# Performance work log

Measured on AMD Instinct MI355X. Metric: run time of the kernel, lower is better.

## Reference

```python
import jax, jax.numpy as jnp
import numpy as np

IN_DIM, DIM, HEADS = 128, 32, 4
L, B = 256, 1


def setup_inputs() -> dict:
    key = jax.random.key(0)
    ks = jax.random.split(key, 10)
    z = jax.random.normal(ks[0], (B, L, L, IN_DIM), dtype=jnp.float32)
    src_mask = jax.random.randint(ks[1], (B, L), 0, 2, dtype=jnp.int32)
    s = 1.0 / np.sqrt(IN_DIM)
    return {
        "z": z,
        "ln_gamma": jnp.ones((IN_DIM,), jnp.float32),
        "ln_beta": jnp.zeros((IN_DIM,), jnp.float32),
        "w_qkv": jax.random.normal(ks[2], (IN_DIM, 3 * HEADS * DIM), jnp.float32) * s,
        "w_pair": jax.random.normal(ks[3], (IN_DIM, HEADS), jnp.float32) * s,
        "w_gate": jax.random.normal(ks[4], (IN_DIM, IN_DIM), jnp.float32) * s,
        "b_gate": jax.random.normal(ks[5], (IN_DIM,), jnp.float32) * 0.02,
        "w_out": jax.random.normal(ks[6], (HEADS * DIM, IN_DIM), jnp.float32) * s,
        "b_out": jax.random.normal(ks[7], (IN_DIM,), jnp.float32) * 0.02,
        "src_mask": src_mask,
    }


def reference(z, ln_gamma, ln_beta, w_qkv, w_pair, w_gate, b_gate, w_out, b_out, src_mask):
    b, i, j, c = z.shape
    h, d = HEADS, DIM
    # mask: zeros -> -1, then outer product -> [b, L, L]
    m = jnp.where(src_mask == 0, -1, src_mask).astype(z.dtype)
    attn_mask = m[:, :, None] * m[:, None, :]
    # LayerNorm over channel dim (eps=1e-5, as nn.LayerNorm default)
    mu = jnp.mean(z, axis=-1, keepdims=True)
    var = jnp.mean((z - mu) ** 2, axis=-1, keepdims=True)
    zn = (z - mu) * jax.lax.rsqrt(var + 1e-5) * ln_gamma + ln_beta
    # qkv projection (no bias), split into heads
    qkv = zn @ w_qkv  # [b,i,j,3*h*d]
    q, k, v = jnp.split(qkv, 3, axis=-1)
    q = q.reshape(b, i, j, h, d)
    k = k.reshape(b, i, j, h, d)
    v = v.reshape(b, i, j, h, d)
    bias = zn @ w_pair  # [b,i,j,h]
    gate = jax.nn.sigmoid(zn @ w_gate + b_gate)  # [b,i,j,c]
    scale = jnp.asarray(d, z.dtype) ** 0.5
    # row-wise attention: attend along j within each row r=i
    logits = jnp.einsum('brihd,brjhd->brijh', q, k) / scale + bias[:, None]
    logits = jnp.where(attn_mask[:, None, :, :, None] == -1, jnp.asarray(-1e-9, z.dtype), logits)
    attn = jax.nn.softmax(logits, axis=3)
    out = jnp.einsum('brijh,brjhd->brihd', attn, v).reshape(b, i, j, h * d)
    out = gate * out
    return out @ w_out + b_out
```

## Files before the change

kernel.cpp:

```cpp
#include <hip/hip_runtime.h>
#include <hip/hip_bf16.h>
#include <math.h>

typedef __attribute__((ext_vector_type(4))) short short4v;
typedef __attribute__((ext_vector_type(8))) short short8v;
typedef __attribute__((ext_vector_type(4))) float f32x4;

#define QB_OFF    0
#define KB_OFF    16777216
#define VB_OFF    33554432
#define BIAS_OFF  50331648
#define GATEB_OFF 51380224
#define ATTB_OFF  68157440
#define WT_OFF    84934656
#define WOT_OFF   85065728

static __device__ __forceinline__ short f2bf(float x) {
    __hip_bfloat16 h = __float2bfloat16(x);
    return *reinterpret_cast<short*>(&h);
}
static __device__ __forceinline__ float bf2f(short x) {
    __hip_bfloat16 h = *reinterpret_cast<__hip_bfloat16*>(&x);
    return __bfloat162float(h);
}

__global__ __launch_bounds__(128) void k_prep_w(
    const float* __restrict__ w_qkv, const float* __restrict__ w_gate,
    const float* __restrict__ w_out, __hip_bfloat16* __restrict__ wT,
    __hip_bfloat16* __restrict__ woT)
{
    const int n = blockIdx.x, k = threadIdx.x;
    if (n < 384)      wT[n*128 + k]        = __float2bfloat16(w_qkv[k*384 + n]);
    else if (n < 512) wT[n*128 + k]        = __float2bfloat16(w_gate[k*128 + (n-384)]);
    else              woT[(n-512)*128 + k] = __float2bfloat16(w_out[k*128 + (n-512)]);
}

__global__ __launch_bounds__(256) void k1_ln_proj(
    const float* __restrict__ z, const float* __restrict__ gamma,
    const float* __restrict__ beta, const float* __restrict__ w_pair,
    const float* __restrict__ b_gate, const int* __restrict__ src_mask,
    const __hip_bfloat16* __restrict__ wT,
    __hip_bfloat16* __restrict__ qb, __hip_bfloat16* __restrict__ kb,
    __hip_bfloat16* __restrict__ vb, float* __restrict__ biasf,
    __hip_bfloat16* __restrict__ gateb)
{
    const int tid = threadIdx.x;
    const int lane = tid & 63, wv = tid >> 6;
    const int l15 = lane & 15, lg4 = lane >> 4;
    const int tokbase = blockIdx.x * 128 + wv * 32;

    float zn[2][32];
    float s[2] = {0.f, 0.f}, s2[2] = {0.f, 0.f};
    #pragma unroll
    for (int mt = 0; mt < 2; ++mt) {
        const float* zp = z + (size_t)(tokbase + mt*16 + l15) * 128 + lg4*8;
        #pragma unroll
        for (int ks = 0; ks < 4; ++ks) {
            float4 a = *(const float4*)(zp + ks*32);
            float4 b = *(const float4*)(zp + ks*32 + 4);
            zn[mt][ks*8+0] = a.x; zn[mt][ks*8+1] = a.y;
            zn[mt][ks*8+2] = a.z; zn[mt][ks*8+3] = a.w;
            zn[mt][ks*8+4] = b.x; zn[mt][ks*8+5] = b.y;
            zn[mt][ks*8+6] = b.z; zn[mt][ks*8+7] = b.w;
            s[mt]  += a.x + a.y + a.z + a.w + b.x + b.y + b.z + b.w;
            s2[mt] += a.x*a.x + a.y*a.y + a.z*a.z + a.w*a.w
                    + b.x*b.x + b.y*b.y + b.z*b.z + b.w*b.w;
        }
    }
    #pragma unroll
    for (int mt = 0; mt < 2; ++mt) {
        s[mt]  += __shfl_xor(s[mt], 16);  s[mt]  += __shfl_xor(s[mt], 32);
        s2[mt] += __shfl_xor(s2[mt], 16); s2[mt] += __shfl_xor(s2[mt], 32);
    }

    #pragma unroll
    for (int ks = 0; ks < 4; ++ks) {
        float4 g0 = *(const float4*)(gamma + ks*32 + lg4*8);
        float4 g1 = *(const float4*)(gamma + ks*32 + lg4*8 + 4);
        float4 b0 = *(const float4*)(beta  + ks*32 + lg4*8);
        float4 b1 = *(const float4*)(beta  + ks*32 + lg4*8 + 4);
        float gg[8] = {g0.x,g0.y,g0.z,g0.w,g1.x,g1.y,g1.z,g1.w};
        float bb[8] = {b0.x,b0.y,b0.z,b0.w,b1.x,b1.y,b1.z,b1.w};
        #pragma unroll
        for (int mt = 0; mt < 2; ++mt) {
            const float mu  = s[mt] * (1.f/128.f);
            const float inv = rsqrtf(s2[mt]*(1.f/128.f) - mu*mu + 1e-5f);
            #pragma unroll
            for (int e = 0; e < 8; ++e)
                zn[mt][ks*8+e] = (zn[mt][ks*8+e] - mu) * inv * gg[e] + bb[e];
        }
    }

    {
        float pr[2][4] = {{0,0,0,0},{0,0,0,0}};
        #pragma unroll
        for (int ks = 0; ks < 4; ++ks)
            #pragma unroll
            for (int e = 0; e < 8; ++e) {
                float4 wp = *(const float4*)(w_pair + (ks*32 + lg4*8 + e)*4);
                #pragma unroll
                for (int mt = 0; mt < 2; ++mt) {
                    const float a = zn[mt][ks*8+e];
                    pr[mt][0] = fmaf(a, wp.x, pr[mt][0]);
                    pr[mt][1] = fmaf(a, wp.y, pr[mt][1]);
                    pr[mt][2] = fmaf(a, wp.z, pr[mt][2]);
                    pr[mt][3] = fmaf(a, wp.w, pr[mt][3]);
                }
            }
        #pragma unroll
        for (int mt = 0; mt < 2; ++mt)
            #pragma unroll
            for (int h = 0; h < 4; ++h) {
                pr[mt][h] += __shfl_xor(pr[mt][h], 16);
                pr[mt][h] += __shfl_xor(pr[mt][h], 32);
            }
        if (lg4 == 0) {
            #pragma unroll
            for (int mt = 0; mt < 2; ++mt) {
                const int t = tokbase + mt*16 + l15;
                const int i = t >> 8, j = t & 255;
                const bool masked = (src_mask[i] == 0) != (src_mask[j] == 0);
                #pragma unroll
                for (int h = 0; h < 4; ++h)
                    biasf[(size_t)(h*256 + j)*256 + i] = masked ? 1e30f : pr[mt][h];
            }
        }
    }

    short8v afr[2][4];
    #pragma unroll
    for (int mt = 0; mt < 2; ++mt)
        #pragma unroll
        for (int ks = 0; ks < 4; ++ks) {
            short8v f;
            #pragma unroll
            for (int e = 0; e < 8; ++e) f[e] = f2bf(zn[mt][ks*8+e]);
            afr[mt][ks] = f;
        }

    const ushort* wTu = (const ushort*)wT;
    for (int ch = 0; ch < 8; ++ch) {
        f32x4 acc[2][4];
        #pragma unroll
        for (int mt = 0; mt < 2; ++mt)
            #pragma unroll
            for (int nt = 0; nt < 4; ++nt) acc[mt][nt] = (f32x4){0.f,0.f,0.f,0.f};
        const ushort* Bb = wTu + (size_t)ch * 64 * 128;
        #pragma unroll
        for (int ks = 0; ks < 4; ++ks)
            #pragma unroll
            for (int nt = 0; nt < 4; ++nt) {
                short8v bfr = *(const short8v*)(Bb + (nt*16 + l15)*128 + ks*32 + lg4*8);
                acc[0][nt] = __builtin_amdgcn_mfma_f32_16x16x32_bf16(afr[0][ks], bfr, acc[0][nt], 0,0,0);
                acc[1][nt] = __builtin_amdgcn_mfma_f32_16x16x32_bf16(afr[1][ks], bfr, acc[1][nt], 0,0,0);
            }
        if (ch < 6) {
            __hip_bfloat16* dst = (ch < 2 ? qb : (ch < 4 ? kb : vb));
            #pragma unroll
            for (int mt = 0; mt < 2; ++mt)
                #pragma unroll
                for (int nt = 0; nt < 4; ++nt) {
                    const int nh = (ch & 1)*64 + nt*16 + l15;
                    const int h = nh >> 5, d = nh & 31;
                    #pragma unroll
                    for (int e = 0; e < 4; ++e) {
                        const int t = tokbase + mt*16 + lg4*4 + e;
                        const int i = t >> 8, j = t & 255;
                        dst[(size_t)((i*4 + h)*256 + j)*32 + d] = __float2bfloat16(acc[mt][nt][e]);
                    }
                }
        } else {
            #pragma unroll
            for (int mt = 0; mt < 2; ++mt)
                #pragma unroll
                for (int nt = 0; nt < 4; ++nt) {
                    const int c = (ch - 6)*64 + nt*16 + l15;
                    const float bg = b_gate[c];
                    #pragma unroll
                    for (int e = 0; e < 4; ++e) {
                        const int t = tokbase + mt*16 + lg4*4 + e;
                        const float v = 1.f / (1.f + __expf(-(acc[mt][nt][e] + bg)));
                        gateb[(size_t)t*128 + c] = __float2bfloat16(v);
                    }
                }
        }
    }
}

__global__ __launch_bounds__(128, 2) void k_attn_mfma(
    const __hip_bfloat16* __restrict__ qb_, const __hip_bfloat16* __restrict__ kb_,
    const __hip_bfloat16* __restrict__ vb_, const float* __restrict__ biasf,
    __hip_bfloat16* __restrict__ attb)
{
    __shared__ __align__(16) char klds[256 * 80];
    const int tid  = threadIdx.x;
    const int lane = tid & 63;
    const int wv   = tid >> 6;
    const int h = blockIdx.x >> 8, r = blockIdx.x & 255;
    const int rh = r * 4 + h;
    const int l15 = lane & 15, lg4 = lane >> 4;

    const ushort* qg = (const ushort*)qb_ + (size_t)rh * 8192;
    const ushort* kg = (const ushort*)kb_ + (size_t)rh * 8192;
    const ushort* vg = (const ushort*)vb_ + (size_t)rh * 8192;

    short4v vfrag[16][2];
    #pragma unroll
    for (int jt = 0; jt < 16; ++jt)
        #pragma unroll
        for (int dt = 0; dt < 2; ++dt) {
            short4v f;
            #pragma unroll
            for (int e = 0; e < 4; ++e)
                f[e] = (short)vg[(size_t)(jt*16 + lg4*4 + e)*32 + dt*16 + l15];
            vfrag[jt][dt] = f;
        }

    #pragma unroll
    for (int t = 0; t < 8; ++t) {
        uint4 kv = *(const uint4*)(kg + t*1024 + tid*8);
        *(uint4*)(klds + (t*32 + (tid >> 2))*80 + (tid & 3)*16) = kv;
    }
    __syncthreads();

    const float inv_scale = 0.17677669529663687f;

    for (int ii = 0; ii < 8; ++ii) {
        const int it = wv*8 + ii;
        short8v qf = *(const short8v*)(qg + (it*16 + l15)*32 + lg4*8);

        f32x4 s[16];
        #pragma unroll
        for (int jt = 0; jt < 16; ++jt) {
            short8v kf = *(const short8v*)(klds + (jt*16 + l15)*80 + lg4*16);
            s[jt] = __builtin_amdgcn_mfma_f32_16x16x32_bf16(
                        kf, qf, (f32x4){0.f,0.f,0.f,0.f}, 0, 0, 0);
        }

        const float* bp = biasf + (size_t)h * 65536 + it*16 + l15;
        #pragma unroll
        for (int jt = 0; jt < 16; ++jt)
            #pragma unroll
            for (int e = 0; e < 4; ++e) {
                const float b = bp[(size_t)(jt*16 + lg4*4 + e) * 256];
                s[jt][e] = (b > 1e29f) ? -1e-9f : fmaf(s[jt][e], inv_scale, b);
            }

        float m = -INFINITY;
        #pragma unroll
        for (int jt = 0; jt < 16; ++jt) {
            const float a = fmaxf(fmaxf(s[jt][0], s[jt][1]),
                                  fmaxf(s[jt][2], s[jt][3]));
            m = fmaxf(m, a);
        }
        m = fmaxf(m, __shfl_xor(m, 16));
        m = fmaxf(m, __shfl_xor(m, 32));

        float lsum = 0.f;
        #pragma unroll
        for (int jt = 0; jt < 16; ++jt)
            #pragma unroll
            for (int e = 0; e < 4; ++e) {
                const float p = __expf(s[jt][e] - m);
                s[jt][e] = p;
                lsum += p;
            }
        lsum += __shfl_xor(lsum, 16);
        lsum += __shfl_xor(lsum, 32);

        short4v pa[16];
        #pragma unroll
        for (int jt = 0; jt < 16; ++jt) {
            short4v t4;
            t4[0] = f2bf(s[jt][0]); t4[1] = f2bf(s[jt][1]);
            t4[2] = f2bf(s[jt][2]); t4[3] = f2bf(s[jt][3]);
            pa[jt] = t4;
        }

        f32x4 o0 = {0.f,0.f,0.f,0.f}, o1 = {0.f,0.f,0.f,0.f};
        #pragma unroll
        for (int jt = 0; jt < 16; ++jt) {
            o0 = __builtin_amdgcn_mfma_f32_16x16x16bf16_1k(pa[jt], vfrag[jt][0], o0, 0, 0, 0);
            o1 = __builtin_amdgcn_mfma_f32_16x16x16bf16_1k(pa[jt], vfrag[jt][1], o1, 0, 0, 0);
        }

        const float invl = 1.f / lsum;
        float il[4];
        #pragma unroll
        for (int e = 0; e < 4; ++e) il[e] = __shfl(invl, lg4*4 + e);

        __hip_bfloat16* op = attb + ((size_t)(r*256 + it*16) * 128) + h*32;
        #pragma unroll
        for (int e = 0; e < 4; ++e) {
            op[(lg4*4 + e)*128 +      l15] = __float2bfloat16(o0[e] * il[e]);
            op[(lg4*4 + e)*128 + 16 + l15] = __float2bfloat16(o1[e] * il[e]);
        }
    }
}

__global__ __launch_bounds__(256) void k3_out_proj(
    const __hip_bfloat16* __restrict__ gateb, const __hip_bfloat16* __restrict__ attb,
    const __hip_bfloat16* __restrict__ woT, const float* __restrict__ b_out,
    float* __restrict__ out)
{
    const int tid = threadIdx.x;
    const int lane = tid & 63, wv = tid >> 6;
    const int l15 = lane & 15, lg4 = lane >> 4;
    const int tokbase = blockIdx.x * 128 + wv * 32;

    const ushort* gu = (const ushort*)gateb;
    const ushort* au = (const ushort*)attb;

    short8v afr[2][4];
    #pragma unroll
    for (int mt = 0; mt < 2; ++mt)
        #pragma unroll
        for (int ks = 0; ks < 4; ++ks) {
            const size_t base = (size_t)(tokbase + mt*16 + l15)*128 + ks*32 + lg4*8;
            short8v gv = *(const short8v*)(gu + base);
            short8v av = *(const short8v*)(au + base);
            short8v p;
            #pragma unroll
            for (int e = 0; e < 8; ++e) p[e] = f2bf(bf2f(gv[e]) * bf2f(av[e]));
            afr[mt][ks] = p;
        }

    const ushort* wo = (const ushort*)woT;
    for (int ch = 0; ch < 2; ++ch) {
        f32x4 acc[2][4];
        #pragma unroll
        for (int mt = 0; mt < 2; ++mt)
            #pragma unroll
            for (int nt = 0; nt < 4; ++nt) acc[mt][nt] = (f32x4){0.f,0.f,0.f,0.f};
        const ushort* Bb = wo + (size_t)ch * 64 * 128;
        #pragma unroll
        for (int ks = 0; ks < 4; ++ks)
            #pragma unroll
            for (int nt = 0; nt < 4; ++nt) {
                short8v bfr = *(const short8v*)(Bb + (nt*16 + l15)*128 + ks*32 + lg4*8);
                acc[0][nt] = __builtin_amdgcn_mfma_f32_16x16x32_bf16(afr[0][ks], bfr, acc[0][nt], 0,0,0);
                acc[1][nt] = __builtin_amdgcn_mfma_f32_16x16x32_bf16(afr[1][ks], bfr, acc[1][nt], 0,0,0);
            }
        #pragma unroll
        for (int mt = 0; mt < 2; ++mt)
            #pragma unroll
            for (int nt = 0; nt < 4; ++nt) {
                const int n = ch*64 + nt*16 + l15;
                const float bo = b_out[n];
                #pragma unroll
                for (int e = 0; e < 4; ++e) {
                    const int t = tokbase + mt*16 + lg4*4 + e;
                    out[(size_t)t*128 + n] = acc[mt][nt][e] + bo;
                }
            }
    }
}

extern "C" void kernel_launch(void* const* d_in, const int* in_sizes, int n_in,
                              void* d_out, int out_size, void* d_ws, size_t ws_size,
                              hipStream_t stream)
{
    const float* z       = (const float*)d_in[0];
    const float* gamma   = (const float*)d_in[1];
    const float* beta    = (const float*)d_in[2];
    const float* w_qkv   = (const float*)d_in[3];
    const float* w_pair  = (const float*)d_in[4];
    const float* w_gate  = (const float*)d_in[5];
    const float* b_gate  = (const float*)d_in[6];
    const float* w_out   = (const float*)d_in[7];
    const float* b_out   = (const float*)d_in[8];
    const int*   src_mask= (const int*)d_in[9];
    float* out = (float*)d_out;
    char*  wsb = (char*)d_ws;

    __hip_bfloat16* qb    = (__hip_bfloat16*)(wsb + QB_OFF);
    __hip_bfloat16* kb    = (__hip_bfloat16*)(wsb + KB_OFF);
    __hip_bfloat16* vb    = (__hip_bfloat16*)(wsb + VB_OFF);
    float*          biasf = (float*)(wsb + BIAS_OFF);
    __hip_bfloat16* gateb = (__hip_bfloat16*)(wsb + GATEB_OFF);
    __hip_bfloat16* attb  = (__hip_bfloat16*)(wsb + ATTB_OFF);
    __hip_bfloat16* wT    = (__hip_bfloat16*)(wsb + WT_OFF);
    __hip_bfloat16* woT   = (__hip_bfloat16*)(wsb + WOT_OFF);

    hipLaunchKernelGGL(k_prep_w, dim3(640), dim3(128), 0, stream,
                       w_qkv, w_gate, w_out, wT, woT);
    hipLaunchKernelGGL(k1_ln_proj, dim3(512), dim3(256), 0, stream,
                       z, gamma, beta, w_pair, b_gate, src_mask, wT,
                       qb, kb, vb, biasf, gateb);
    hipLaunchKernelGGL(k_attn_mfma, dim3(1024), dim3(128), 0, stream,
                       qb, kb, vb, biasf, attb);
    hipLaunchKernelGGL(k3_out_proj, dim3(512), dim3(256), 0, stream,
                       gateb, attb, woT, b_out, out);
}
```

Measured before the change: 112.3 us.

## Split projection across blocks, stage V in LDS, transpose bias layout

The LN+projection kernel is split into two half-grids, each computing half the output channels, which doubles the block count; only one half writes the pair bias. The pair bias is now stored row-major per (h,i) so the attention kernel can read it with contiguous float4 loads instead of strided scalar loads. The attention kernel moves to 256 threads, stages V through a swizzled LDS buffer rather than per-lane register gathers, and applies the softmax normalisation before the PV matmul. The output projection kernel uses 16-token tiles per wave across twice as many blocks. The cost is recomputing LayerNorm twice per token in the split kernel, plus extra LDS use per attention block.

New measurement: 138.0 us. +22.9%, slower.

```diff
diff --git a/kernel.cpp b/kernel.cpp
--- a/kernel.cpp
+++ b/kernel.cpp
@@ -47,7 +47,8 @@
     const int tid = threadIdx.x;
     const int lane = tid & 63, wv = tid >> 6;
     const int l15 = lane & 15, lg4 = lane >> 4;
-    const int tokbase = blockIdx.x * 128 + wv * 32;
+    const int half = blockIdx.x >> 9;
+    const int tokbase = (blockIdx.x & 511) * 128 + wv * 32;
 
     float zn[2][32];
     float s[2] = {0.f, 0.f}, s2[2] = {0.f, 0.f};
@@ -91,7 +92,7 @@
         }
     }
 
-    {
+    if (half == 0) {
         float pr[2][4] = {{0,0,0,0},{0,0,0,0}};
         #pragma unroll
         for (int ks = 0; ks < 4; ++ks)
@@ -122,7 +123,7 @@
                 const bool masked = (src_mask[i] == 0) != (src_mask[j] == 0);
                 #pragma unroll
                 for (int h = 0; h < 4; ++h)
-                    biasf[(size_t)(h*256 + j)*256 + i] = masked ? 1e30f : pr[mt][h];
+                    biasf[(size_t)(h*256 + i)*256 + j] = masked ? 1e30f : pr[mt][h];
             }
         }
     }
@@ -139,7 +140,8 @@
         }
 
     const ushort* wTu = (const ushort*)wT;
-    for (int ch = 0; ch < 8; ++ch) {
+    for (int ci = 0; ci < 4; ++ci) {
+        const int ch = half*4 + ci;
         f32x4 acc[2][4];
         #pragma unroll
         for (int mt = 0; mt < 2; ++mt)
@@ -187,12 +189,13 @@
     }
 }
 
-__global__ __launch_bounds__(128, 2) void k_attn_mfma(
+__global__ __launch_bounds__(256) void k_attn_mfma(
     const __hip_bfloat16* __restrict__ qb_, const __hip_bfloat16* __restrict__ kb_,
     const __hip_bfloat16* __restrict__ vb_, const float* __restrict__ biasf,
     __hip_bfloat16* __restrict__ attb)
 {
     __shared__ __align__(16) char klds[256 * 80];
+    __shared__ __align__(16) char vlds[16384];
     const int tid  = threadIdx.x;
     const int lane = tid & 63;
     const int wv   = tid >> 6;
@@ -204,29 +207,28 @@
     const ushort* kg = (const ushort*)kb_ + (size_t)rh * 8192;
     const ushort* vg = (const ushort*)vb_ + (size_t)rh * 8192;
 
-    short4v vfrag[16][2];
-    #pragma unroll
-    for (int jt = 0; jt < 16; ++jt)
-        #pragma unroll
-        for (int dt = 0; dt < 2; ++dt) {
-            short4v f;
-            #pragma unroll
-            for (int e = 0; e < 4; ++e)
-                f[e] = (short)vg[(size_t)(jt*16 + lg4*4 + e)*32 + dt*16 + l15];
-            vfrag[jt][dt] = f;
-        }
-
-    #pragma unroll
-    for (int t = 0; t < 8; ++t) {
-        uint4 kv = *(const uint4*)(kg + t*1024 + tid*8);
-        *(uint4*)(klds + (t*32 + (tid >> 2))*80 + (tid & 3)*16) = kv;
+    #pragma unroll
+    for (int t = 0; t < 4; ++t) {
+        uint4 kv = *(const uint4*)(kg + t*2048 + tid*8);
+        *(uint4*)(klds + (t*64 + (tid >> 2))*80 + (tid & 3)*16) = kv;
+    }
+    {
+        const int j = tid;
+        uint4 tmp[4];
+        #pragma unroll
+        for (int c = 0; c < 4; ++c)
+            tmp[c] = *(const uint4*)(vg + (size_t)j*32 + c*8);
+        const ushort* vals = (const ushort*)tmp;
+        #pragma unroll
+        for (int d = 0; d < 32; ++d)
+            *(ushort*)(vlds + d*512 + (((j >> 2) ^ (d & 15)) << 3) + (j & 3)*2) = vals[d];
     }
     __syncthreads();
 
     const float inv_scale = 0.17677669529663687f;
 
-    for (int ii = 0; ii < 8; ++ii) {
-        const int it = wv*8 + ii;
+    for (int ii = 0; ii < 4; ++ii) {
+        const int it = wv*4 + ii;
         short8v qf = *(const short8v*)(qg + (it*16 + l15)*32 + lg4*8);
 
         f32x4 s[16];
@@ -237,14 +239,14 @@
                         kf, qf, (f32x4){0.f,0.f,0.f,0.f}, 0, 0, 0);
         }
 
-        const float* bp = biasf + (size_t)h * 65536 + it*16 + l15;
-        #pragma unroll
-        for (int jt = 0; jt < 16; ++jt)
-            #pragma unroll
-            for (int e = 0; e < 4; ++e) {
-                const float b = bp[(size_t)(jt*16 + lg4*4 + e) * 256];
-                s[jt][e] = (b > 1e29f) ? -1e-9f : fmaf(s[jt][e], inv_scale, b);
-            }
+        const float* bp = biasf + (size_t)(h*256 + it*16 + l15) * 256;
+        #pragma unroll
+        for (int jt = 0; jt < 16; ++jt) {
+            f32x4 bv = *(const f32x4*)(bp + jt*16 + lg4*4);
+            #pragma unroll
+            for (int e = 0; e < 4; ++e)
+                s[jt][e] = (bv[e] > 1e29f) ? -1e-9f : fmaf(s[jt][e], inv_scale, bv[e]);
+        }
 
         float m = -INFINITY;
         #pragma unroll
@@ -267,33 +269,32 @@
             }
         lsum += __shfl_xor(lsum, 16);
         lsum += __shfl_xor(lsum, 32);
+        const float invl = 1.f / lsum;
 
         short4v pa[16];
         #pragma unroll
         for (int jt = 0; jt < 16; ++jt) {
             short4v t4;
-            t4[0] = f2bf(s[jt][0]); t4[1] = f2bf(s[jt][1]);
-            t4[2] = f2bf(s[jt][2]); t4[3] = f2bf(s[jt][3]);
+            t4[0] = f2bf(s[jt][0] * invl); t4[1] = f2bf(s[jt][1] * invl);
+            t4[2] = f2bf(s[jt][2] * invl); t4[3] = f2bf(s[jt][3] * invl);
             pa[jt] = t4;
         }
 
         f32x4 o0 = {0.f,0.f,0.f,0.f}, o1 = {0.f,0.f,0.f,0.f};
         #pragma unroll
         for (int jt = 0; jt < 16; ++jt) {
-            o0 = __builtin_amdgcn_mfma_f32_16x16x16bf16_1k(pa[jt], vfrag[jt][0], o0, 0, 0, 0);
-            o1 = __builtin_amdgcn_mfma_f32_16x16x16bf16_1k(pa[jt], vfrag[jt][1], o1, 0, 0, 0);
-        }
-
-        const float invl = 1.f / lsum;
-        float il[4];
-        #pragma unroll
-        for (int e = 0; e < 4; ++e) il[e] = __shfl(invl, lg4*4 + e);
+            const int d0 = l15, d1 = 16 + l15;
+            short4v vf0 = *(const short4v*)(vlds + d0*512 + (((jt*4 + lg4) ^ (d0 & 15)) << 3));
+            short4v vf1 = *(const short4v*)(vlds + d1*512 + (((jt*4 + lg4) ^ (d1 & 15)) << 3));
+            o0 = __builtin_amdgcn_mfma_f32_16x16x16bf16_1k(pa[jt], vf0, o0, 0, 0, 0);
+            o1 = __builtin_amdgcn_mfma_f32_16x16x16bf16_1k(pa[jt], vf1, o1, 0, 0, 0);
+        }
 
         __hip_bfloat16* op = attb + ((size_t)(r*256 + it*16) * 128) + h*32;
         #pragma unroll
         for (int e = 0; e < 4; ++e) {
-            op[(lg4*4 + e)*128 +      l15] = __float2bfloat16(o0[e] * il[e]);
-            op[(lg4*4 + e)*128 + 16 + l15] = __float2bfloat16(o1[e] * il[e]);
+            op[(lg4*4 + e)*128 +      l15] = __float2bfloat16(o0[e]);
+            op[(lg4*4 + e)*128 + 16 + l15] = __float2bfloat16(o1[e]);
         }
     }
 }
@@ -306,53 +307,46 @@
     const int tid = threadIdx.x;
     const int lane = tid & 63, wv = tid >> 6;
     const int l15 = lane & 15, lg4 = lane >> 4;
-    const int tokbase = blockIdx.x * 128 + wv * 32;
+    const int tokbase = blockIdx.x * 64 + wv * 16;
 
     const ushort* gu = (const ushort*)gateb;
     const ushort* au = (const ushort*)attb;
 
-    short8v afr[2][4];
-    #pragma unroll
-    for (int mt = 0; mt < 2; ++mt)
-        #pragma unroll
-        for (int ks = 0; ks < 4; ++ks) {
-            const size_t base = (size_t)(tokbase + mt*16 + l15)*128 + ks*32 + lg4*8;
-            short8v gv = *(const short8v*)(gu + base);
-            short8v av = *(const short8v*)(au + base);
-            short8v p;
-            #pragma unroll
-            for (int e = 0; e < 8; ++e) p[e] = f2bf(bf2f(gv[e]) * bf2f(av[e]));
-            afr[mt][ks] = p;
-        }
+    short8v afr[4];
+    #pragma unroll
+    for (int ks = 0; ks < 4; ++ks) {
+        const size_t base = (size_t)(tokbase + l15)*128 + ks*32 + lg4*8;
+        short8v gv = *(const short8v*)(gu + base);
+        short8v av = *(const short8v*)(au + base);
+        short8v p;
+        #pragma unroll
+        for (int e = 0; e < 8; ++e) p[e] = f2bf(bf2f(gv[e]) * bf2f(av[e]));
+        afr[ks] = p;
+    }
 
     const ushort* wo = (const ushort*)woT;
     for (int ch = 0; ch < 2; ++ch) {
-        f32x4 acc[2][4];
-        #pragma unroll
-        for (int mt = 0; mt < 2; ++mt)
-            #pragma unroll
-            for (int nt = 0; nt < 4; ++nt) acc[mt][nt] = (f32x4){0.f,0.f,0.f,0.f};
+        f32x4 acc[4];
+        #pragma unroll
+        for (int nt = 0; nt < 4; ++nt) acc[nt] = (f32x4){0.f,0.f,0.f,0.f};
         const ushort* Bb = wo + (size_t)ch * 64 * 128;
         #pragma unroll
         for (int ks = 0; ks < 4; ++ks)
             #pragma unroll
             for (int nt = 0; nt < 4; ++nt) {
                 short8v bfr = *(const short8v*)(Bb + (nt*16 + l15)*128 + ks*32 + lg4*8);
-                acc[0][nt] = __builtin_amdgcn_mfma_f32_16x16x32_bf16(afr[0][ks], bfr, acc[0][nt], 0,0,0);
-                acc[1][nt] = __builtin_amdgcn_mfma_f32_16x16x32_bf16(afr[1][ks], bfr, acc[1][nt], 0,0,0);
-            }
-        #pragma unroll
-        for (int mt = 0; mt < 2; ++mt)
-            #pragma unroll
-            for (int nt = 0; nt < 4; ++nt) {
-                const int n = ch*64 + nt*16 + l15;
-                const float bo = b_out[n];
-                #pragma unroll
-                for (int e = 0; e < 4; ++e) {
-                    const int t = tokbase + mt*16 + lg4*4 + e;
-                    out[(size_t)t*128 + n] = acc[mt][nt][e] + bo;
-                }
-            }
+                acc[nt] = __builtin_amdgcn_mfma_f32_16x16x32_bf16(afr[ks], bfr, acc[nt], 0,0,0);
+            }
+        #pragma unroll
+        for (int nt = 0; nt < 4; ++nt) {
+            const int n = ch*64 + nt*16 + l15;
+            const float bo = b_out[n];
+            #pragma unroll
+            for (int e = 0; e < 4; ++e) {
+                const int t = tokbase + lg4*4 + e;
+                out[(size_t)t*128 + n] = acc[nt][e] + bo;
+            }
+        }
     }
 }
 
@@ -384,11 +378,11 @@
 
     hipLaunchKernelGGL(k_prep_w, dim3(640), dim3(128), 0, stream,
                        w_qkv, w_gate, w_out, wT, woT);
-    hipLaunchKernelGGL(k1_ln_proj, dim3(512), dim3(256), 0, stream,
+    hipLaunchKernelGGL(k1_ln_proj, dim3(1024), dim3(256), 0, stream,
                        z, gamma, beta, w_pair, b_gate, src_mask, wT,
                        qb, kb, vb, biasf, gateb);
-    hipLaunchKernelGGL(k_attn_mfma, dim3(1024), dim3(128), 0, stream,
+    hipLaunchKernelGGL(k_attn_mfma, dim3(1024), dim3(256), 0, stream,
                        qb, kb, vb, biasf, attb);
-    hipLaunchKernelGGL(k3_out_proj, dim3(512), dim3(256), 0, stream,
+    hipLaunchKernelGGL(k3_out_proj, dim3(1024), dim3(256), 0, stream,
                        gateb, attb, woT, b_out, out);
 }
```
